# Kernel optimization log

Hardware: AMD Instinct MI355X
Metric: run time of the kernel (lower is better)

The kernel has to match this reference:

```python
import jax, jax.numpy as jnp
import numpy as np

IN_DIM, OUT_DIM, NUM, K = 64, 16, 5, 3
BATCH = 65536


def extend_grid(grid, k):
    # grid: (in_dim, num+1) uniform; append k points on each side with step h
    h = (grid[:, -1:] - grid[:, :1]) / (grid.shape[1] - 1)
    left = grid[:, :1] - h * jnp.arange(k, 0, -1, dtype=grid.dtype)
    right = grid[:, -1:] + h * jnp.arange(1, k + 1, dtype=grid.dtype)
    return jnp.concatenate([left, grid, right], axis=1)  # (in_dim, num+2k+1)


def b_batch(x, grid, k):
    # Cox-de Boor recursion. x: (B, in_dim), grid: (in_dim, G+2k+1)
    xe = x[:, :, None]          # (B, in, 1)
    g = grid[None, :, :]        # (1, in, G+2k+1)
    B = ((xe >= g[:, :, :-1]) & (xe < g[:, :, 1:])).astype(x.dtype)
    for p in range(1, k + 1):
        B = ((xe - g[:, :, :-(p + 1)]) / (g[:, :, p:-1] - g[:, :, :-(p + 1)]) * B[:, :, :-1]
             + (g[:, :, p + 1:] - xe) / (g[:, :, p + 1:] - g[:, :, 1:-p]) * B[:, :, 1:])
        B = jnp.nan_to_num(B)
    return B  # (B, in, G+k)


def setup_inputs() -> dict:
    key = jax.random.key(0)
    k1, k2, k3 = jax.random.split(key, 3)
    x = jax.random.normal(k1, (BATCH, IN_DIM), dtype=jnp.float32)
    base_grid = jnp.broadcast_to(jnp.linspace(-1.0, 1.0, NUM + 1, dtype=jnp.float32), (IN_DIM, NUM + 1))
    grid = extend_grid(base_grid, K)                       # (in, num+2k+1)
    coef = jax.random.normal(k2, (IN_DIM, OUT_DIM, NUM + K), dtype=jnp.float32) * 0.1
    scale_sp = jnp.ones((IN_DIM, OUT_DIM), dtype=jnp.float32) / np.sqrt(IN_DIM).astype(np.float32)
    scale_base = (jax.random.uniform(k3, (IN_DIM, OUT_DIM), dtype=jnp.float32) * 2.0 - 1.0) / np.sqrt(IN_DIM).astype(np.float32)
    return {"x": x, "grid": grid, "coef": coef, "scale_base": scale_base, "scale_sp": scale_sp}


def reference(x, grid, coef, scale_base, scale_sp):
    bs = x.shape[0]
    preacts = jnp.broadcast_to(x[:, None, :], (bs, OUT_DIM, IN_DIM))
    B = b_batch(x, grid, K)                                # (bs, in, G+k)
    y = jnp.einsum('bik,iok->bio', B, coef)                # coef2curve: (bs, in, out)
    postspline = jnp.transpose(y, (0, 2, 1))               # (bs, out, in)
    base = jax.nn.silu(x)                                  # SiLU base function (include_bias=True)
    y = scale_base[None, :, :] * base[:, :, None] + scale_sp[None, :, :] * y
    postacts = jnp.transpose(y, (0, 2, 1))                 # (bs, out, in)
    out = jnp.sum(y, axis=1)                               # (bs, out)
    return (out, preacts, postacts, postspline)
```

## Files before the change

### kernel.cpp

```cpp
#include <hip/hip_runtime.h>

#define IN_DIM 64
#define OUT_DIM 16
#define NGRID 12
#define NB 8
#define TST 68
#define ROWS 8

typedef _Float16 half2_t __attribute__((ext_vector_type(2)));
typedef float    fx4     __attribute__((ext_vector_type(4)));

__device__ __forceinline__ half2_t pkrtz(float a, float b) {
    return __builtin_bit_cast(half2_t, __builtin_amdgcn_cvt_pkrtz(a, b));
}

__device__ __forceinline__ float dpp_add16(float v) {
    int x = __builtin_bit_cast(int, v);
    v += __builtin_bit_cast(float, __builtin_amdgcn_update_dpp(0, x, 0x118, 0xf, 0xf, true));
    x = __builtin_bit_cast(int, v);
    v += __builtin_bit_cast(float, __builtin_amdgcn_update_dpp(0, x, 0x114, 0xf, 0xf, true));
    x = __builtin_bit_cast(int, v);
    v += __builtin_bit_cast(float, __builtin_amdgcn_update_dpp(0, x, 0x112, 0xf, 0xf, true));
    x = __builtin_bit_cast(int, v);
    v += __builtin_bit_cast(float, __builtin_amdgcn_update_dpp(0, x, 0x111, 0xf, 0xf, true));
    return v;
}

__global__ __launch_bounds__(256, 3) void kan_fwd_kernel(
    const float* __restrict__ x,
    const float* __restrict__ grid,
    const float* __restrict__ coef,
    const float* __restrict__ sbase,
    const float* __restrict__ ssp,
    float* __restrict__ out,
    float* __restrict__ preacts,
    float* __restrict__ postacts,
    float* __restrict__ postspline,
    int batch)
{
    __shared__ float sT[4][OUT_DIM * TST];

    const int bid = blockIdx.x;
    const int tid = threadIdx.x;

    if (bid % 3 == 2) {
        const int fb = bid / 3;
        const fx4* __restrict__ xv = reinterpret_cast<const fx4*>(x);
        const size_t base = (size_t)fb * 16384;
        #pragma unroll 4
        for (int s = 0; s < 64; ++s) {
            const size_t q = base + (size_t)s * 256 + tid;
            const fx4 v = xv[(q >> 8) * 16 + (q & 15)];
            __builtin_nontemporal_store(v, reinterpret_cast<fx4*>(&preacts[4 * q]));
        }
        return;
    }

    const int mb = (bid / 3) * 2 + (bid % 3);
    const int lane = tid & 63;
    const int wave = tid >> 6;
    const int i = lane;

    const long b0 = ((long)mb * 4 + wave) * ROWS;
    if (b0 >= batch) return;

    const float g0 = grid[i * NGRID + 0];
    const float g1 = grid[i * NGRID + 1];
    const float invh = 1.0f / (g1 - g0);

    half2_t c[OUT_DIM][4];
    {
        const fx4* c4 = reinterpret_cast<const fx4*>(coef + (size_t)i * OUT_DIM * NB);
        #pragma unroll
        for (int o = 0; o < OUT_DIM; ++o) {
            fx4 a = c4[o * 2], bq = c4[o * 2 + 1];
            c[o][0] = pkrtz(a.x,  a.y);
            c[o][1] = pkrtz(a.z,  a.w);
            c[o][2] = pkrtz(bq.x, bq.y);
            c[o][3] = pkrtz(bq.z, bq.w);
        }
    }

    const int ci = (lane & 15) * 4;
    const int ro = lane >> 4;
    float sbt[4][4], spt[4][4];
    #pragma unroll
    for (int sl = 0; sl < 4; ++sl) {
        const int o = sl * 4 + ro;
        #pragma unroll
        for (int k = 0; k < 4; ++k) {
            sbt[sl][k] = sbase[(ci + k) * OUT_DIM + o];
            spt[sl][k] = ssp  [(ci + k) * OUT_DIM + o];
        }
    }

    float* sTw = sT[wave];
    float xi_cur = x[b0 * IN_DIM + i];

    #pragma unroll 1
    for (int r = 0; r < ROWS; ++r) {
        const long b = b0 + r;
        if (b >= batch) break;
        float xi_next = 0.0f;
        if (r + 1 < ROWS && b + 1 < batch) xi_next = x[(b + 1) * IN_DIM + i];
        const float xi = xi_cur;

        const float t = (xi - g0) * invh;
        float d[NGRID];
        #pragma unroll
        for (int j = 0; j < NGRID; ++j) d[j] = t - (float)j;

        float Bv[11];
        #pragma unroll
        for (int j = 0; j < 11; ++j)
            Bv[j] = (d[j] >= 0.0f && d[j + 1] < 0.0f) ? 1.0f : 0.0f;

        #pragma unroll
        for (int j = 0; j < 10; ++j)
            Bv[j] = d[j] * Bv[j] - d[j + 2] * Bv[j + 1];
        #pragma unroll
        for (int j = 0; j < 9; ++j)
            Bv[j] = (d[j] * Bv[j] - d[j + 3] * Bv[j + 1]) * 0.5f;
        #pragma unroll
        for (int j = 0; j < 8; ++j)
            Bv[j] = (d[j] * Bv[j] - d[j + 4] * Bv[j + 1]) * (1.0f / 3.0f);

        half2_t bh[4];
        #pragma unroll
        for (int q = 0; q < 4; ++q)
            bh[q] = pkrtz(Bv[2 * q], Bv[2 * q + 1]);

        #pragma unroll
        for (int o = 0; o < OUT_DIM; ++o) {
            float y = __builtin_amdgcn_fdot2(c[o][0], bh[0],
                      __builtin_amdgcn_fdot2(c[o][1], bh[1],
                      __builtin_amdgcn_fdot2(c[o][2], bh[2],
                      __builtin_amdgcn_fdot2(c[o][3], bh[3], 0.0f, false),
                      false), false), false);
            sTw[o * TST + i] = y;
        }

        const float base = xi / (1.0f + __expf(-xi));
        fx4 bq;
        bq.x = __shfl(base, ci + 0, 64);
        bq.y = __shfl(base, ci + 1, 64);
        bq.z = __shfl(base, ci + 2, 64);
        bq.w = __shfl(base, ci + 3, 64);

        const size_t rowoff = (size_t)b * (OUT_DIM * IN_DIM);
        float ps0, ps1, ps2, ps3;

        #pragma unroll
        for (int sl = 0; sl < 4; ++sl) {
            const int row = sl * 4 + ro;
            fx4 yv = *reinterpret_cast<const fx4*>(&sTw[row * TST + ci]);
            fx4 y2;
            y2.x = __builtin_fmaf(sbt[sl][0], bq.x, spt[sl][0] * yv.x);
            y2.y = __builtin_fmaf(sbt[sl][1], bq.y, spt[sl][1] * yv.y);
            y2.z = __builtin_fmaf(sbt[sl][2], bq.z, spt[sl][2] * yv.z);
            y2.w = __builtin_fmaf(sbt[sl][3], bq.w, spt[sl][3] * yv.w);

            const size_t goff = rowoff + (size_t)sl * 256 + 4 * lane;
            __builtin_nontemporal_store(yv, reinterpret_cast<fx4*>(&postspline[goff]));
            __builtin_nontemporal_store(y2, reinterpret_cast<fx4*>(&postacts[goff]));

            const float ps = (y2.x + y2.y) + (y2.z + y2.w);
            if (sl == 0) ps0 = ps; else if (sl == 1) ps1 = ps;
            else if (sl == 2) ps2 = ps; else ps3 = ps;
        }

        ps0 = dpp_add16(ps0);
        ps1 = dpp_add16(ps1);
        ps2 = dpp_add16(ps2);
        ps3 = dpp_add16(ps3);
        if ((lane & 15) == 15) {
            float* ob = out + (size_t)b * OUT_DIM;
            ob[0  + ro] = ps0;
            ob[4  + ro] = ps1;
            ob[8  + ro] = ps2;
            ob[12 + ro] = ps3;
        }

        xi_cur = xi_next;
    }
}

extern "C" void kernel_launch(void* const* d_in, const int* in_sizes, int n_in,
                              void* d_out, int out_size, void* d_ws, size_t ws_size,
                              hipStream_t stream) {
    const float* x     = (const float*)d_in[0];
    const float* grid  = (const float*)d_in[1];
    const float* coef  = (const float*)d_in[2];
    const float* sbase = (const float*)d_in[3];
    const float* ssp   = (const float*)d_in[4];

    const int batch = in_sizes[0] / IN_DIM;

    float* out = (float*)d_out;
    float* preacts    = out + (size_t)batch * OUT_DIM;
    float* postacts   = preacts  + (size_t)batch * OUT_DIM * IN_DIM;
    float* postspline = postacts + (size_t)batch * OUT_DIM * IN_DIM;

    const int nblocks = 3072;
    kan_fwd_kernel<<<nblocks, 256, 0, stream>>>(
        x, grid, coef, sbase, ssp, out, preacts, postacts, postspline, batch);
}
```

Before: 168.3 us.

## Split fused KAN kernel into separate spline, activations, and preacts kernels

Replaces the single fused kernel, which interleaved preacts-copy blocks with compute blocks, with three kernels launched in sequence: one writes postspline, one recomputes the spline and writes postacts and out, and one broadcasts x into preacts. The aim is simpler per-kernel store streams and less per-block register and store pressure. In exchange the B-spline basis and dot products are computed twice, and three launches run serially, so the copy no longer overlaps with compute.

```diff
diff --git a/kernel.cpp b/kernel.cpp
--- a/kernel.cpp
+++ b/kernel.cpp
@@ -26,47 +26,42 @@
     return v;
 }
 
-__global__ __launch_bounds__(256, 3) void kan_fwd_kernel(
-    const float* __restrict__ x,
-    const float* __restrict__ grid,
-    const float* __restrict__ coef,
-    const float* __restrict__ sbase,
-    const float* __restrict__ ssp,
-    float* __restrict__ out,
-    float* __restrict__ preacts,
-    float* __restrict__ postacts,
-    float* __restrict__ postspline,
-    int batch)
+__device__ __forceinline__ void spline_basis(float t, half2_t bh[4]) {
+    float d[NGRID];
+    #pragma unroll
+    for (int j = 0; j < NGRID; ++j) d[j] = t - (float)j;
+
+    float Bv[11];
+    #pragma unroll
+    for (int j = 0; j < 11; ++j)
+        Bv[j] = (d[j] >= 0.0f && d[j + 1] < 0.0f) ? 1.0f : 0.0f;
+
+    #pragma unroll
+    for (int j = 0; j < 10; ++j)
+        Bv[j] = d[j] * Bv[j] - d[j + 2] * Bv[j + 1];
+    #pragma unroll
+    for (int j = 0; j < 9; ++j)
+        Bv[j] = (d[j] * Bv[j] - d[j + 3] * Bv[j + 1]) * 0.5f;
+    #pragma unroll
+    for (int j = 0; j < 8; ++j)
+        Bv[j] = (d[j] * Bv[j] - d[j + 4] * Bv[j + 1]) * (1.0f / 3.0f);
+
+    #pragma unroll
+    for (int q = 0; q < 4; ++q)
+        bh[q] = pkrtz(Bv[2 * q], Bv[2 * q + 1]);
+}
+
+__global__ __launch_bounds__(256, 3) void kan_spline_kernel(
+    const float* __restrict__ x, const float* __restrict__ grid,
+    const float* __restrict__ coef, float* __restrict__ postspline, int batch)
 {
     __shared__ float sT[4][OUT_DIM * TST];
-
-    const int bid = blockIdx.x;
-    const int tid = threadIdx.x;
-
-    if (bid % 3 == 2) {
-        const int fb = bid / 3;
-        const fx4* __restrict__ xv = reinterpret_cast<const fx4*>(x);
-        const size_t base = (size_t)fb * 16384;
-        #pragma unroll 4
-        for (int s = 0; s < 64; ++s) {
-            const size_t q = base + (size_t)s * 256 + tid;
-            const fx4 v = xv[(q >> 8) * 16 + (q & 15)];
-            __builtin_nontemporal_store(v, reinterpret_cast<fx4*>(&preacts[4 * q]));
-        }
-        return;
-    }
-
-    const int mb = (bid / 3) * 2 + (bid % 3);
-    const int lane = tid & 63;
-    const int wave = tid >> 6;
-    const int i = lane;
-
-    const long b0 = ((long)mb * 4 + wave) * ROWS;
+    const int tid = threadIdx.x, lane = tid & 63, wave = tid >> 6, i = lane;
+    const long b0 = ((long)blockIdx.x * 4 + wave) * ROWS;
     if (b0 >= batch) return;
 
     const float g0 = grid[i * NGRID + 0];
-    const float g1 = grid[i * NGRID + 1];
-    const float invh = 1.0f / (g1 - g0);
+    const float invh = 1.0f / (grid[i * NGRID + 1] - g0);
 
     half2_t c[OUT_DIM][4];
     {
@@ -74,10 +69,70 @@
         #pragma unroll
         for (int o = 0; o < OUT_DIM; ++o) {
             fx4 a = c4[o * 2], bq = c4[o * 2 + 1];
-            c[o][0] = pkrtz(a.x,  a.y);
-            c[o][1] = pkrtz(a.z,  a.w);
-            c[o][2] = pkrtz(bq.x, bq.y);
-            c[o][3] = pkrtz(bq.z, bq.w);
+            c[o][0] = pkrtz(a.x, a.y);  c[o][1] = pkrtz(a.z, a.w);
+            c[o][2] = pkrtz(bq.x, bq.y); c[o][3] = pkrtz(bq.z, bq.w);
+        }
+    }
+
+    const int ci = (lane & 15) * 4;
+    const int ro = lane >> 4;
+    float* sTw = sT[wave];
+    float xi_cur = x[b0 * IN_DIM + i];
+
+    #pragma unroll 1
+    for (int r = 0; r < ROWS; ++r) {
+        const long b = b0 + r;
+        float xi_next = 0.0f;
+        if (r + 1 < ROWS && b + 1 < batch) xi_next = x[(b + 1) * IN_DIM + i];
+        const float t = (xi_cur - g0) * invh;
+
+        half2_t bh[4];
+        spline_basis(t, bh);
+
+        #pragma unroll
+        for (int o = 0; o < OUT_DIM; ++o) {
+            float y = __builtin_amdgcn_fdot2(c[o][0], bh[0],
+                      __builtin_amdgcn_fdot2(c[o][1], bh[1],
+                      __builtin_amdgcn_fdot2(c[o][2], bh[2],
+                      __builtin_amdgcn_fdot2(c[o][3], bh[3], 0.0f, false),
+                      false), false), false);
+            sTw[o * TST + i] = y;
+        }
+
+        const size_t rowoff = (size_t)b * (OUT_DIM * IN_DIM);
+        #pragma unroll
+        for (int sl = 0; sl < 4; ++sl) {
+            const int row = sl * 4 + ro;
+            fx4 yv = *reinterpret_cast<const fx4*>(&sTw[row * TST + ci]);
+            __builtin_nontemporal_store(yv,
+                reinterpret_cast<fx4*>(&postspline[rowoff + (size_t)sl * 256 + 4 * lane]));
+        }
+        xi_cur = xi_next;
+    }
+}
+
+__global__ __launch_bounds__(256, 3) void kan_acts_kernel(
+    const float* __restrict__ x, const float* __restrict__ grid,
+    const float* __restrict__ coef, const float* __restrict__ sbase,
+    const float* __restrict__ ssp, float* __restrict__ out,
+    float* __restrict__ postacts, int batch)
+{
+    __shared__ float sT[4][OUT_DIM * TST];
+    const int tid = threadIdx.x, lane = tid & 63, wave = tid >> 6, i = lane;
+    const long b0 = ((long)blockIdx.x * 4 + wave) * ROWS;
+    if (b0 >= batch) return;
+
+    const float g0 = grid[i * NGRID + 0];
+    const float invh = 1.0f / (grid[i * NGRID + 1] - g0);
+
+    half2_t c[OUT_DIM][4];
+    {
+        const fx4* c4 = reinterpret_cast<const fx4*>(coef + (size_t)i * OUT_DIM * NB);
+        #pragma unroll
+        for (int o = 0; o < OUT_DIM; ++o) {
+            fx4 a = c4[o * 2], bq = c4[o * 2 + 1];
+            c[o][0] = pkrtz(a.x, a.y);  c[o][1] = pkrtz(a.z, a.w);
+            c[o][2] = pkrtz(bq.x, bq.y); c[o][3] = pkrtz(bq.z, bq.w);
         }
     }
 
@@ -100,35 +155,13 @@
     #pragma unroll 1
     for (int r = 0; r < ROWS; ++r) {
         const long b = b0 + r;
-        if (b >= batch) break;
         float xi_next = 0.0f;
         if (r + 1 < ROWS && b + 1 < batch) xi_next = x[(b + 1) * IN_DIM + i];
         const float xi = xi_cur;
-
         const float t = (xi - g0) * invh;
-        float d[NGRID];
-        #pragma unroll
-        for (int j = 0; j < NGRID; ++j) d[j] = t - (float)j;
-
-        float Bv[11];
-        #pragma unroll
-        for (int j = 0; j < 11; ++j)
-            Bv[j] = (d[j] >= 0.0f && d[j + 1] < 0.0f) ? 1.0f : 0.0f;
-
-        #pragma unroll
-        for (int j = 0; j < 10; ++j)
-            Bv[j] = d[j] * Bv[j] - d[j + 2] * Bv[j + 1];
-        #pragma unroll
-        for (int j = 0; j < 9; ++j)
-            Bv[j] = (d[j] * Bv[j] - d[j + 3] * Bv[j + 1]) * 0.5f;
-        #pragma unroll
-        for (int j = 0; j < 8; ++j)
-            Bv[j] = (d[j] * Bv[j] - d[j + 4] * Bv[j + 1]) * (1.0f / 3.0f);
 
         half2_t bh[4];
-        #pragma unroll
-        for (int q = 0; q < 4; ++q)
-            bh[q] = pkrtz(Bv[2 * q], Bv[2 * q + 1]);
+        spline_basis(t, bh);
 
         #pragma unroll
         for (int o = 0; o < OUT_DIM; ++o) {
@@ -160,9 +193,8 @@
             y2.z = __builtin_fmaf(sbt[sl][2], bq.z, spt[sl][2] * yv.z);
             y2.w = __builtin_fmaf(sbt[sl][3], bq.w, spt[sl][3] * yv.w);
 
-            const size_t goff = rowoff + (size_t)sl * 256 + 4 * lane;
-            __builtin_nontemporal_store(yv, reinterpret_cast<fx4*>(&postspline[goff]));
-            __builtin_nontemporal_store(y2, reinterpret_cast<fx4*>(&postacts[goff]));
+            __builtin_nontemporal_store(y2,
+                reinterpret_cast<fx4*>(&postacts[rowoff + (size_t)sl * 256 + 4 * lane]));
 
             const float ps = (y2.x + y2.y) + (y2.z + y2.w);
             if (sl == 0) ps0 = ps; else if (sl == 1) ps1 = ps;
@@ -180,8 +212,33 @@
             ob[8  + ro] = ps2;
             ob[12 + ro] = ps3;
         }
-
         xi_cur = xi_next;
+    }
+}
+
+__global__ __launch_bounds__(256) void kan_pre_kernel(
+    const float* __restrict__ x, float* __restrict__ preacts, int batch)
+{
+    const int lane = threadIdx.x & 63;
+    const int wave = threadIdx.x >> 6;
+    const long b0 = ((long)blockIdx.x * 4 + wave) * 16;
+    if (b0 >= batch) return;
+    const fx4* __restrict__ xv = reinterpret_cast<const fx4*>(x);
+    fx4* __restrict__ pa = reinterpret_cast<fx4*>(preacts);
+    const int col = lane & 15;
+
+    fx4 v = xv[b0 * 16 + col];
+    #pragma unroll 1
+    for (int r = 0; r < 16; ++r) {
+        const long b = b0 + r;
+        fx4 vn = v;
+        if (r + 1 < 16 && b + 1 < batch) vn = xv[(b + 1) * 16 + col];
+        const long base = b * 256;
+        __builtin_nontemporal_store(v, &pa[base +   0 + lane]);
+        __builtin_nontemporal_store(v, &pa[base +  64 + lane]);
+        __builtin_nontemporal_store(v, &pa[base + 128 + lane]);
+        __builtin_nontemporal_store(v, &pa[base + 192 + lane]);
+        v = vn;
     }
 }
 
@@ -201,7 +258,10 @@
     float* postacts   = preacts  + (size_t)batch * OUT_DIM * IN_DIM;
     float* postspline = postacts + (size_t)batch * OUT_DIM * IN_DIM;
 
-    const int nblocks = 3072;
-    kan_fwd_kernel<<<nblocks, 256, 0, stream>>>(
-        x, grid, coef, sbase, ssp, out, preacts, postacts, postspline, batch);
-}
+    const int nb_main = (batch + 4 * ROWS - 1) / (4 * ROWS);
+    const int nb_pre  = (batch + 4 * 16 - 1) / (4 * 16);
+
+    kan_spline_kernel<<<nb_main, 256, 0, stream>>>(x, grid, coef, postspline, batch);
+    kan_acts_kernel  <<<nb_main, 256, 0, stream>>>(x, grid, coef, sbase, ssp, out, postacts, batch);
+    kan_pre_kernel   <<<nb_pre,  256, 0, stream>>>(x, preacts, batch);
+}
```

Result: slower. 190.9 us (+13.4%).
